# Kernel tuning notes

Measured on AMD Instinct MI355X. Metric: run time of the kernel, lower is better.

Reference implementation:

```python
import jax, jax.numpy as jnp
import numpy as np

N = 50000        # nodes
N_EDGES = 800000 # edges before self loops
D_IN = 128       # in_features
D_OUT = 64       # out_features (per head)
H = 2            # heads
NEG_SLOPE = 0.2  # GATv2Conv default negative_slope
EPS = 1e-5       # LayerNorm eps


def setup_inputs() -> dict:
    key = jax.random.key(0)
    ks = jax.random.split(key, 8)
    X = jax.random.normal(ks[0], (N, D_IN), jnp.float32)
    E = jax.random.randint(ks[1], (2, N_EDGES), 0, N, dtype=jnp.int32)
    attr = jax.random.normal(ks[2], (N_EDGES,), jnp.float32)
    # GATv2Conv params: lin_l / lin_r (share_weights=False, bias=True), att, concat bias
    s_in = 1.0 / np.sqrt(D_IN)
    W_l = jax.random.normal(ks[3], (D_IN, H * D_OUT), jnp.float32) * s_in
    b_l = jnp.zeros((H * D_OUT,), jnp.float32)
    W_r = jax.random.normal(ks[4], (D_IN, H * D_OUT), jnp.float32) * s_in
    b_r = jnp.zeros((H * D_OUT,), jnp.float32)
    att = jax.random.normal(ks[5], (H, D_OUT), jnp.float32) * (1.0 / np.sqrt(D_OUT))
    bias = jnp.zeros((H * D_OUT,), jnp.float32)
    # final_linear + LayerNorm params
    W_f = jax.random.normal(ks[6], (H * D_OUT, D_OUT), jnp.float32) * (1.0 / np.sqrt(H * D_OUT))
    b_f = jnp.zeros((D_OUT,), jnp.float32)
    gamma = jnp.ones((D_OUT,), jnp.float32)
    beta = jnp.zeros((D_OUT,), jnp.float32)
    return dict(X=X, E=E, attr=attr, W_l=W_l, b_l=b_l, W_r=W_r, b_r=b_r,
                att=att, bias=bias, W_f=W_f, b_f=b_f, gamma=gamma, beta=beta)


def _forward(X, E, W_l, b_l, W_r, b_r, att, bias, W_f, b_f, gamma, beta):
    # add self loops (PyG GATv2Conv default add_self_loops=True)
    loop = jnp.arange(N, dtype=E.dtype)
    src = jnp.concatenate([E[0], loop])  # [Et]
    dst = jnp.concatenate([E[1], loop])  # [Et]
    x_l = (X @ W_l + b_l).reshape(N, H, D_OUT)  # source-side transform
    x_r = (X @ W_r + b_r).reshape(N, H, D_OUT)  # target-side transform
    # per-edge GATv2 score: a^T LeakyReLU(x_i + x_j)
    s = jax.nn.leaky_relu(x_l[src] + x_r[dst], NEG_SLOPE)      # [Et, H, C]
    alpha = jnp.einsum('ehc,hc->eh', s, att)                   # [Et, H]
    # segment softmax over incoming edges of each target node
    a_max = jax.ops.segment_max(alpha, dst, num_segments=N)    # [N, H]
    a_max = jnp.where(jnp.isfinite(a_max), a_max, 0.0)
    num = jnp.exp(alpha - a_max[dst])
    den = jax.ops.segment_sum(num, dst, num_segments=N)
    w = num / den[dst]                                         # [Et, H]
    # weighted scatter-aggregate of source messages
    out = jax.ops.segment_sum(x_l[src] * w[:, :, None], dst, num_segments=N)  # [N,H,C]
    out = out.reshape(N, H * D_OUT) + bias                     # concat heads + bias
    # final linear + LayerNorm
    h = out @ W_f + b_f                                        # [N, D_OUT]
    mu = jnp.mean(h, axis=-1, keepdims=True)
    var = jnp.mean((h - mu) ** 2, axis=-1, keepdims=True)
    return (h - mu) * jax.lax.rsqrt(var + EPS) * gamma + beta


def reference(X, E, attr, W_l, b_l, W_r, b_r, att, bias, W_f, b_f, gamma, beta):
    H_out = _forward(X, E, W_l, b_l, W_r, b_r, att, bias, W_f, b_f, gamma, beta)
    return (H_out, E, attr)
```

## Files before the change

### kernel.cpp

```cpp
#include <hip/hip_runtime.h>

typedef unsigned short u16;
typedef unsigned int   u32;


#define DIN   128
#define DOUT  64
#define HD    128
#define BCAP  64

typedef __attribute__((ext_vector_type(8))) _Float16 f16x8;
typedef __attribute__((ext_vector_type(2))) _Float16 h2;
typedef __attribute__((ext_vector_type(4))) float    f32x4;

union H2U { u32 u; h2 h; };
__device__ __forceinline__ h2  U2H(u32 u) { H2U x; x.u = u; return x.h; }
__device__ __forceinline__ u32 H2Ub(h2 h) { H2U x; x.h = h; return x.u; }

__device__ __forceinline__ u16 f2h(float f) {
    _Float16 h = (_Float16)f;
    u16 r; __builtin_memcpy(&r, &h, 2); return r;
}

__device__ __forceinline__ u32 pkmax(u32 a, u32 b) {
    u32 d;
    asm("v_pk_max_f16 %0, %1, %2" : "=v"(d) : "v"(a), "v"(b));
    return d;
}

__device__ __forceinline__ float fdot2f(h2 a, h2 b, float c) {
#if __has_builtin(__builtin_amdgcn_fdot2)
    return __builtin_amdgcn_fdot2(a, b, c, false);
#else
    return c + (float)a[0] * (float)b[0] + (float)a[1] * (float)b[1];
#endif
}

__global__ void prep_small(const float* __restrict__ Wl, const float* __restrict__ Wr,
                           const float* __restrict__ Wf,
                           u16* __restrict__ WTl, u16* __restrict__ WTr,
                           uint4* __restrict__ Wfp, int* __restrict__ count, int N)
{
    int i = blockIdx.x * 256 + threadIdx.x;
    if (i < N) { count[i] = 0; return; }
    int j = i - N;
    if (j < 16384) {
        int k = j >> 7, c = j & 127;
        WTl[c * 128 + k] = f2h(Wl[j]);
    } else if (j < 32768) {
        int t = j - 16384;
        int k = t >> 7, c = t & 127;
        WTr[c * 128 + k] = f2h(Wr[t]);
    } else if (j < 33792) {
        int t = j - 32768;
        int k4 = t >> 5, c = t & 31;
        const float* wrow = Wf + (size_t)(4 * k4) * DOUT;
        u32 a0 = (u32)f2h(wrow[c])              | ((u32)f2h(wrow[DOUT + c]) << 16);
        u32 a1 = (u32)f2h(wrow[2 * DOUT + c])   | ((u32)f2h(wrow[3 * DOUT + c]) << 16);
        u32 a2 = (u32)f2h(wrow[c + 32])         | ((u32)f2h(wrow[DOUT + c + 32]) << 16);
        u32 a3 = (u32)f2h(wrow[2 * DOUT + c + 32]) | ((u32)f2h(wrow[3 * DOUT + c + 32]) << 16);
        Wfp[t] = make_uint4(a0, a1, a2, a3);
    }
}

__global__ void edge_prep(const int* __restrict__ E, const float* __restrict__ attr,
                          int* __restrict__ count, u16* __restrict__ bucket,
                          float* __restrict__ out, int N, int NE)
{
    int i = blockIdx.x * 256 + threadIdx.x;
    if (i < NE) {
        int src = E[i];
        int dst = E[NE + i];
        if ((u32)dst >= (u32)N) dst = 0;
        if ((u32)src >= (u32)N) src = 0;
        int rank = atomicAdd(&count[dst], 1);
        if (rank < BCAP) bucket[(size_t)dst * BCAP + rank] = (u16)src;
    } else {
        int j = i - NE;
        const size_t base = (size_t)N * DOUT;
        if (j < 2 * NE) {
            out[base + j] = (float)E[j];
        } else {
            int t = j - 2 * NE;
            if (t < NE) out[base + 2 * (size_t)NE + t] = attr[t];
        }
    }
}

__global__ __launch_bounds__(256) void gemm1(
    const float* __restrict__ X,
    const u16* __restrict__ WTl, const float* __restrict__ bl,
    const u16* __restrict__ WTr, const float* __restrict__ br,
    u16* __restrict__ xl_p, u16* __restrict__ xr_p, int N)
{
    __shared__ u16 sX[64 * 136];
    __shared__ u16 sW[128 * 136];

    const int tid  = threadIdx.x;
    const int row0 = blockIdx.x * 64;
    const int cb   = blockIdx.y;
    const u16*   WT  = (cb == 0) ? WTl : WTr;
    const float* bia = (cb == 0) ? bl : br;

    for (int idx = tid; idx < 64 * 32; idx += 256) {
        int r  = idx >> 5;
        int k4 = (idx & 31) << 2;
        int gr = row0 + r;
        float4 v = make_float4(0.f, 0.f, 0.f, 0.f);
        if (gr < N) v = *(const float4*)(X + (size_t)gr * DIN + k4);
        u32 p0 = (u32)f2h(v.x) | ((u32)f2h(v.y) << 16);
        u32 p1 = (u32)f2h(v.z) | ((u32)f2h(v.w) << 16);
        *(uint2*)&sX[r * 136 + k4] = make_uint2(p0, p1);
    }
    for (int idx = tid; idx < 128 * 16; idx += 256) {
        int c  = idx >> 4;
        int k8 = (idx & 15) << 3;
        *(uint4*)&sW[c * 136 + k8] = *(const uint4*)&WT[c * 128 + k8];
    }
    __syncthreads();

    const int wv   = tid >> 6;
    const int lane = tid & 63;
    const int m    = lane & 15;
    const int quad = lane >> 4;

    f32x4 acc[8] = {};
    #pragma unroll
    for (int kc = 0; kc < 4; kc++) {
        f16x8 bx = *(const f16x8*)&sX[(wv * 16 + m) * 136 + kc * 32 + quad * 8];
        #pragma unroll
        for (int t = 0; t < 8; t++) {
            f16x8 aw = *(const f16x8*)&sW[(t * 16 + m) * 136 + kc * 32 + quad * 8];
            acc[t] = __builtin_amdgcn_mfma_f32_16x16x32_f16(aw, bx, acc[t], 0, 0, 0);
        }
    }

    const int gn = row0 + wv * 16 + m;
    if (gn < N) {
        u16* dst = (cb == 0) ? xl_p : xr_p;
        #pragma unroll
        for (int t = 0; t < 8; t++) {
            const int c0 = t * 16 + quad * 4;
            float4 bv = *(const float4*)(bia + c0);
            u32 p0 = (u32)f2h(acc[t][0] + bv.x) | ((u32)f2h(acc[t][1] + bv.y) << 16);
            u32 p1 = (u32)f2h(acc[t][2] + bv.z) | ((u32)f2h(acc[t][3] + bv.w) << 16);
            *(uint2*)(dst + (size_t)gn * HD + c0) = make_uint2(p0, p1);
        }
    }
}

template<int D>
__device__ __forceinline__ void edge_block(
    int myidx, int j, int sgbase, const char* xbase,
    const h2* xr2, const h2* at2, h2 c02,
    h2* acc2, float& lden)
{
    uint4 q[D];
    #pragma unroll
    for (int b = 0; b < D; b++) {
        u32 off = (u32)__shfl(myidx, sgbase + j + 2 * b) << 8;
        q[b] = *(const uint4*)(xbase + off);
    }
    float sh[D];
    #pragma unroll
    for (int b = 0; b < D; b++) {
        h2 v0 = U2H(q[b].x) + xr2[0];
        h2 v1 = U2H(q[b].y) + xr2[1];
        h2 v2 = U2H(q[b].z) + xr2[2];
        h2 v3 = U2H(q[b].w) + xr2[3];
        v0 = U2H(pkmax(H2Ub(v0), H2Ub(v0 * c02)));
        v1 = U2H(pkmax(H2Ub(v1), H2Ub(v1 * c02)));
        v2 = U2H(pkmax(H2Ub(v2), H2Ub(v2 * c02)));
        v3 = U2H(pkmax(H2Ub(v3), H2Ub(v3 * c02)));
        float s = fdot2f(v0, at2[0], 0.f);
        s = fdot2f(v1, at2[1], s);
        s = fdot2f(v2, at2[2], s);
        s = fdot2f(v3, at2[3], s);
        sh[b] = s;
    }
    #pragma unroll
    for (int m = 4; m; m >>= 1) {
        #pragma unroll
        for (int b = 0; b < D; b++) sh[b] += __shfl_xor(sh[b], m);
    }
    #pragma unroll
    for (int b = 0; b < D; b++) {
        float p = exp2f(sh[b]);
        lden += p;
        _Float16 ph = (_Float16)p;
        h2 p2 = {ph, ph};
        acc2[0] += p2 * U2H(q[b].x);
        acc2[1] += p2 * U2H(q[b].y);
        acc2[2] += p2 * U2H(q[b].z);
        acc2[3] += p2 * U2H(q[b].w);
    }
}

__global__ __launch_bounds__(256, 8) void edge_fused(
    const u16* __restrict__ xl_p, const u16* __restrict__ xr_p,
    const float* __restrict__ att, const float* __restrict__ bias,
    const uint4* __restrict__ Wfp, const float* __restrict__ bf,
    const float* __restrict__ gamma, const float* __restrict__ beta,
    const int* __restrict__ count, const u16* __restrict__ bucket,
    float* __restrict__ out, int N)
{
    __shared__ uint4 sWp[32 * 32];
    __shared__ u32   sAggU[8 * 64];

    const int tid = threadIdx.x;
    for (int idx = tid; idx < 1024; idx += 256) sWp[idx] = Wfp[idx];
    __syncthreads();

    const int l      = tid & 63;
    const int half   = tid >> 5;
    const int hl     = tid & 31;
    const int g16    = l & 15;
    const int ch0    = g16 * 8;
    const int sgsel  = (l >> 4) & 1;
    const int sgbase = (l & 32) + sgsel;
    const int n      = blockIdx.x * 8 + half;
    const bool active = (n < N);

    const h2 c02 = {(_Float16)0.2f, (_Float16)0.2f};
    h2 at2[4], xr2[4];
    {
        const float L2E = 1.44269504f;
        float4 a0 = *(const float4*)(att + ch0);
        float4 a1 = *(const float4*)(att + ch0 + 4);
        at2[0] = h2{(_Float16)(a0.x * L2E), (_Float16)(a0.y * L2E)};
        at2[1] = h2{(_Float16)(a0.z * L2E), (_Float16)(a0.w * L2E)};
        at2[2] = h2{(_Float16)(a1.x * L2E), (_Float16)(a1.y * L2E)};
        at2[3] = h2{(_Float16)(a1.z * L2E), (_Float16)(a1.w * L2E)};
        uint4 pr = make_uint4(0, 0, 0, 0);
        if (active) pr = *(const uint4*)(xr_p + (size_t)n * HD + ch0);
        xr2[0] = U2H(pr.x); xr2[1] = U2H(pr.y);
        xr2[2] = U2H(pr.z); xr2[3] = U2H(pr.w);
    }

    h2 acc2[4] = {};
    float lden = 0.f;

    int cnt_b = 0;
    if (active) {
        cnt_b = count[n];
        if (cnt_b < 0) cnt_b = 0;
        if (cnt_b > BCAP) cnt_b = BCAP;
    }
    const int cnt = active ? cnt_b + 1 : 0;
    const u16* mybkt = bucket + (size_t)(active ? n : 0) * BCAP;

    const char* xbase = (const char*)xl_p + ch0 * 2;

    int done = 0;
    while (done < cnt) {
        int chunk = cnt - done; if (chunk > 32) chunk = 32;
        int myidx = 0;
        if (hl < chunk) {
            int gj = done + hl;
            myidx = (gj < cnt_b) ? (int)mybkt[gj] : n;
        }
        int j = 0;
        for (; j + 16 <= chunk; j += 16)
            edge_block<8>(myidx, j, sgbase, xbase, xr2, at2, c02, acc2, lden);
        if (j + 8 <= chunk) {
            edge_block<4>(myidx, j, sgbase, xbase, xr2, at2, c02, acc2, lden);
            j += 8;
        }
        if (j + 4 <= chunk) {
            edge_block<2>(myidx, j, sgbase, xbase, xr2, at2, c02, acc2, lden);
            j += 4;
        }
        for (; j < chunk; j += 2) {
            u32 off = (u32)__shfl(myidx, sgbase + j) << 8;
            uint4 q = *(const uint4*)(xbase + off);
            h2 v0 = U2H(q.x) + xr2[0];
            h2 v1 = U2H(q.y) + xr2[1];
            h2 v2 = U2H(q.z) + xr2[2];
            h2 v3 = U2H(q.w) + xr2[3];
            v0 = U2H(pkmax(H2Ub(v0), H2Ub(v0 * c02)));
            v1 = U2H(pkmax(H2Ub(v1), H2Ub(v1 * c02)));
            v2 = U2H(pkmax(H2Ub(v2), H2Ub(v2 * c02)));
            v3 = U2H(pkmax(H2Ub(v3), H2Ub(v3 * c02)));
            float s = fdot2f(v0, at2[0], 0.f);
            s = fdot2f(v1, at2[1], s);
            s = fdot2f(v2, at2[2], s);
            s = fdot2f(v3, at2[3], s);
            #pragma unroll
            for (int m = 4; m; m >>= 1) s += __shfl_xor(s, m);
            float p = (j + sgsel < chunk) ? exp2f(s) : 0.f;
            lden += p;
            _Float16 ph = (_Float16)p;
            h2 p2 = {ph, ph};
            acc2[0] += p2 * U2H(q.x);
            acc2[1] += p2 * U2H(q.y);
            acc2[2] += p2 * U2H(q.z);
            acc2[3] += p2 * U2H(q.w);
        }
        done += chunk;
    }

    #pragma unroll
    for (int i = 0; i < 4; i++) {
        u32 o = (u32)__shfl_xor((int)H2Ub(acc2[i]), 16);
        acc2[i] = acc2[i] + U2H(o);
    }
    lden += __shfl_xor(lden, 16);

    float rl = 1.f / fmaxf(lden, 1e-30f);
    if (!(l & 16)) {
        float4 b0 = *(const float4*)(bias + ch0);
        float4 b1 = *(const float4*)(bias + ch0 + 4);
        uint4 w;
        w.x = (u32)f2h((float)acc2[0][0] * rl + b0.x) |
              ((u32)f2h((float)acc2[0][1] * rl + b0.y) << 16);
        w.y = (u32)f2h((float)acc2[1][0] * rl + b0.z) |
              ((u32)f2h((float)acc2[1][1] * rl + b0.w) << 16);
        w.z = (u32)f2h((float)acc2[2][0] * rl + b1.x) |
              ((u32)f2h((float)acc2[2][1] * rl + b1.y) << 16);
        w.w = (u32)f2h((float)acc2[3][0] * rl + b1.z) |
              ((u32)f2h((float)acc2[3][1] * rl + b1.w) << 16);
        *(uint4*)&sAggU[half * 64 + g16 * 4] = w;
    }
    asm volatile("s_waitcnt lgkmcnt(0)" ::: "memory");

    float h0 = bf[hl], h1 = bf[hl + 32];
    #pragma unroll 8
    for (int k4 = 0; k4 < 32; k4++) {
        uint4 wp = sWp[k4 * 32 + hl];
        uint2 ag = *(const uint2*)&sAggU[half * 64 + k4 * 2];
        h0 = fdot2f(U2H(ag.x), U2H(wp.x), h0);
        h0 = fdot2f(U2H(ag.y), U2H(wp.y), h0);
        h1 = fdot2f(U2H(ag.x), U2H(wp.z), h1);
        h1 = fdot2f(U2H(ag.y), U2H(wp.w), h1);
    }

    float s1r = h0 + h1, s2r = h0 * h0 + h1 * h1;
    #pragma unroll
    for (int m = 16; m; m >>= 1) { s1r += __shfl_xor(s1r, m); s2r += __shfl_xor(s2r, m); }
    float mu  = s1r * (1.f / 64.f);
    float var = s2r * (1.f / 64.f) - mu * mu;
    float rs  = rsqrtf(fmaxf(var, 0.f) + 1e-5f);
    if (active) {
        out[(size_t)n * DOUT + hl]      = (h0 - mu) * rs * gamma[hl]      + beta[hl];
        out[(size_t)n * DOUT + hl + 32] = (h1 - mu) * rs * gamma[hl + 32] + beta[hl + 32];
    }
}

extern "C" void kernel_launch(void* const* d_in, const int* in_sizes, int n_in,
                              void* d_out, int out_size, void* d_ws, size_t ws_size,
                              hipStream_t stream) {
    const float* X    = (const float*)d_in[0];
    const int*   E    = (const int*)d_in[1];
    const float* attr = (const float*)d_in[2];
    const float* Wl   = (const float*)d_in[3];
    const float* bl   = (const float*)d_in[4];
    const float* Wr   = (const float*)d_in[5];
    const float* br   = (const float*)d_in[6];
    const float* att  = (const float*)d_in[7];
    const float* bias = (const float*)d_in[8];
    const float* Wf   = (const float*)d_in[9];
    const float* bf   = (const float*)d_in[10];
    const float* gamma= (const float*)d_in[11];
    const float* beta = (const float*)d_in[12];
    float* out = (float*)d_out;

    const int N  = in_sizes[0] / DIN;
    const int NE = in_sizes[1] / 2;

    char* ws = (char*)d_ws;
    int* count      = (int*)ws;               ws += (size_t)N * 4;
    u16* bucket     = (u16*)ws;               ws += (size_t)N * BCAP * 2;
    u16* xl_p       = (u16*)ws;               ws += (size_t)N * HD * 2;
    u16* xr_p       = (u16*)ws;               ws += (size_t)N * HD * 2;
    u16* WTl        = (u16*)ws;               ws += 128 * 128 * 2;
    u16* WTr        = (u16*)ws;               ws += 128 * 128 * 2;
    uint4* Wfp      = (uint4*)ws;             ws += 1024 * 16;

    prep_small<<<(N + 33792 + 255) / 256, 256, 0, stream>>>(
        Wl, Wr, Wf, WTl, WTr, Wfp, count, N);

    edge_prep<<<(4 * NE + 255) / 256, 256, 0, stream>>>(
        E, attr, count, bucket, out, N, NE);

    gemm1<<<dim3((N + 63) / 64, 2), 256, 0, stream>>>(X, WTl, bl, WTr, br, xl_p, xr_p, N);

    edge_fused<<<(N + 7) / 8, 256, 0, stream>>>(
        xl_p, xr_p, att, bias, Wfp, bf, gamma, beta,
        count, bucket, out, N);
}
```

Before: 223.1 us.

## Split edge scatter into destination-range passes, merge gemm halves, drop LDS weights

The edge bucket scatter now runs as four launches, each handling only edges whose destination falls in one quarter of the node range. The intent is to keep atomic counters and bucket writes within a cache-resident region, at the cost of reading the edge list four times. The output copy of E/attr moves into the prep kernel. gemm1 now computes both the left and right projections in one block, reusing the X tile and reading weights straight from global memory instead of staging them in LDS. The edge kernel's occupancy hint is lowered from 8 to 6 blocks per CU.

```diff
diff --git a/kernel.cpp b/kernel.cpp
--- a/kernel.cpp
+++ b/kernel.cpp
@@ -8,6 +8,7 @@
 #define DOUT  64
 #define HD    128
 #define BCAP  64
+#define NSEG  4
 
 typedef __attribute__((ext_vector_type(8))) _Float16 f16x8;
 typedef __attribute__((ext_vector_type(2))) _Float16 h2;
@@ -36,10 +37,12 @@
 #endif
 }
 
-__global__ void prep_small(const float* __restrict__ Wl, const float* __restrict__ Wr,
-                           const float* __restrict__ Wf,
-                           u16* __restrict__ WTl, u16* __restrict__ WTr,
-                           uint4* __restrict__ Wfp, int* __restrict__ count, int N)
+__global__ void k_prep(const float* __restrict__ Wl, const float* __restrict__ Wr,
+                       const float* __restrict__ Wf, const int* __restrict__ E,
+                       const float* __restrict__ attr,
+                       u16* __restrict__ WTl, u16* __restrict__ WTr,
+                       uint4* __restrict__ Wfp, int* __restrict__ count,
+                       float* __restrict__ out, int N, int NE)
 {
     int i = blockIdx.x * 256 + threadIdx.x;
     if (i < N) { count[i] = 0; return; }
@@ -60,31 +63,26 @@
         u32 a2 = (u32)f2h(wrow[c + 32])         | ((u32)f2h(wrow[DOUT + c + 32]) << 16);
         u32 a3 = (u32)f2h(wrow[2 * DOUT + c + 32]) | ((u32)f2h(wrow[3 * DOUT + c + 32]) << 16);
         Wfp[t] = make_uint4(a0, a1, a2, a3);
-    }
-}
-
-__global__ void edge_prep(const int* __restrict__ E, const float* __restrict__ attr,
-                          int* __restrict__ count, u16* __restrict__ bucket,
-                          float* __restrict__ out, int N, int NE)
-{
-    int i = blockIdx.x * 256 + threadIdx.x;
-    if (i < NE) {
-        int src = E[i];
-        int dst = E[NE + i];
-        if ((u32)dst >= (u32)N) dst = 0;
-        if ((u32)src >= (u32)N) src = 0;
-        int rank = atomicAdd(&count[dst], 1);
-        if (rank < BCAP) bucket[(size_t)dst * BCAP + rank] = (u16)src;
     } else {
-        int j = i - NE;
+        int p = j - 33792;
         const size_t base = (size_t)N * DOUT;
-        if (j < 2 * NE) {
-            out[base + j] = (float)E[j];
-        } else {
-            int t = j - 2 * NE;
-            if (t < NE) out[base + 2 * (size_t)NE + t] = attr[t];
-        }
-    }
+        if (p < 2 * NE)      out[base + p] = (float)E[p];
+        else if (p < 3 * NE) out[base + p] = attr[p - 2 * NE];
+    }
+}
+
+__global__ void k_scatter(const int* __restrict__ E, int* __restrict__ count,
+                          u16* __restrict__ bucket, int N, int NE, int lo, int hi)
+{
+    int e = blockIdx.x * 256 + threadIdx.x;
+    if (e >= NE) return;
+    int dst = E[NE + e];
+    if ((u32)dst >= (u32)N) dst = 0;
+    if (dst < lo || dst >= hi) return;
+    int src = E[e];
+    if ((u32)src >= (u32)N) src = 0;
+    int rank = atomicAdd(&count[dst], 1);
+    if (rank < BCAP) bucket[(size_t)dst * BCAP + rank] = (u16)src;
 }
 
 __global__ __launch_bounds__(256) void gemm1(
@@ -94,13 +92,9 @@
     u16* __restrict__ xl_p, u16* __restrict__ xr_p, int N)
 {
     __shared__ u16 sX[64 * 136];
-    __shared__ u16 sW[128 * 136];
 
     const int tid  = threadIdx.x;
     const int row0 = blockIdx.x * 64;
-    const int cb   = blockIdx.y;
-    const u16*   WT  = (cb == 0) ? WTl : WTr;
-    const float* bia = (cb == 0) ? bl : br;
 
     for (int idx = tid; idx < 64 * 32; idx += 256) {
         int r  = idx >> 5;
@@ -112,11 +106,6 @@
         u32 p1 = (u32)f2h(v.z) | ((u32)f2h(v.w) << 16);
         *(uint2*)&sX[r * 136 + k4] = make_uint2(p0, p1);
     }
-    for (int idx = tid; idx < 128 * 16; idx += 256) {
-        int c  = idx >> 4;
-        int k8 = (idx & 15) << 3;
-        *(uint4*)&sW[c * 136 + k8] = *(const uint4*)&WT[c * 128 + k8];
-    }
     __syncthreads();
 
     const int wv   = tid >> 6;
@@ -124,27 +113,36 @@
     const int m    = lane & 15;
     const int quad = lane >> 4;
 
-    f32x4 acc[8] = {};
-    #pragma unroll
-    for (int kc = 0; kc < 4; kc++) {
-        f16x8 bx = *(const f16x8*)&sX[(wv * 16 + m) * 136 + kc * 32 + quad * 8];
+    f16x8 bx[4];
+    #pragma unroll
+    for (int kc = 0; kc < 4; kc++)
+        bx[kc] = *(const f16x8*)&sX[(wv * 16 + m) * 136 + kc * 32 + quad * 8];
+
+    const int gn = row0 + wv * 16 + m;
+
+    #pragma unroll
+    for (int cb = 0; cb < 2; cb++) {
+        const u16*   WT  = cb ? WTr : WTl;
+        const float* bia = cb ? br  : bl;
+        f32x4 acc[8] = {};
         #pragma unroll
-        for (int t = 0; t < 8; t++) {
-            f16x8 aw = *(const f16x8*)&sW[(t * 16 + m) * 136 + kc * 32 + quad * 8];
-            acc[t] = __builtin_amdgcn_mfma_f32_16x16x32_f16(aw, bx, acc[t], 0, 0, 0);
-        }
-    }
-
-    const int gn = row0 + wv * 16 + m;
-    if (gn < N) {
-        u16* dst = (cb == 0) ? xl_p : xr_p;
-        #pragma unroll
-        for (int t = 0; t < 8; t++) {
-            const int c0 = t * 16 + quad * 4;
-            float4 bv = *(const float4*)(bia + c0);
-            u32 p0 = (u32)f2h(acc[t][0] + bv.x) | ((u32)f2h(acc[t][1] + bv.y) << 16);
-            u32 p1 = (u32)f2h(acc[t][2] + bv.z) | ((u32)f2h(acc[t][3] + bv.w) << 16);
-            *(uint2*)(dst + (size_t)gn * HD + c0) = make_uint2(p0, p1);
+        for (int kc = 0; kc < 4; kc++) {
+            #pragma unroll
+            for (int t = 0; t < 8; t++) {
+                f16x8 aw = *(const f16x8*)&WT[(t * 16 + m) * 128 + kc * 32 + quad * 8];
+                acc[t] = __builtin_amdgcn_mfma_f32_16x16x32_f16(aw, bx[kc], acc[t], 0, 0, 0);
+            }
+        }
+        if (gn < N) {
+            u16* dst = cb ? xr_p : xl_p;
+            #pragma unroll
+            for (int t = 0; t < 8; t++) {
+                const int c0 = t * 16 + quad * 4;
+                float4 bv = *(const float4*)(bia + c0);
+                u32 p0 = (u32)f2h(acc[t][0] + bv.x) | ((u32)f2h(acc[t][1] + bv.y) << 16);
+                u32 p1 = (u32)f2h(acc[t][2] + bv.z) | ((u32)f2h(acc[t][3] + bv.w) << 16);
+                *(uint2*)(dst + (size_t)gn * HD + c0) = make_uint2(p0, p1);
+            }
         }
     }
 }
@@ -196,7 +194,7 @@
     }
 }
 
-__global__ __launch_bounds__(256, 8) void edge_fused(
+__global__ __launch_bounds__(256, 6) void k_edge(
     const u16* __restrict__ xl_p, const u16* __restrict__ xr_p,
     const float* __restrict__ att, const float* __restrict__ bias,
     const uint4* __restrict__ Wfp, const float* __restrict__ bf,
@@ -204,7 +202,7 @@
     const int* __restrict__ count, const u16* __restrict__ bucket,
     float* __restrict__ out, int N)
 {
-    __shared__ uint4 sWp[32 * 32];
+    __shared__ uint4 sWp[1024];
     __shared__ u32   sAggU[8 * 64];
 
     const int tid = threadIdx.x;
@@ -366,6 +364,7 @@
 
     const int N  = in_sizes[0] / DIN;
     const int NE = in_sizes[1] / 2;
+    const int GB = (N + 63) / 64;
 
     char* ws = (char*)d_ws;
     int* count      = (int*)ws;               ws += (size_t)N * 4;
@@ -376,15 +375,19 @@
     u16* WTr        = (u16*)ws;               ws += 128 * 128 * 2;
     uint4* Wfp      = (uint4*)ws;             ws += 1024 * 16;
 
-    prep_small<<<(N + 33792 + 255) / 256, 256, 0, stream>>>(
-        Wl, Wr, Wf, WTl, WTr, Wfp, count, N);
-
-    edge_prep<<<(4 * NE + 255) / 256, 256, 0, stream>>>(
-        E, attr, count, bucket, out, N, NE);
-
-    gemm1<<<dim3((N + 63) / 64, 2), 256, 0, stream>>>(X, WTl, bl, WTr, br, xl_p, xr_p, N);
-
-    edge_fused<<<(N + 7) / 8, 256, 0, stream>>>(
-        xl_p, xr_p, att, bias, Wfp, bf, gamma, beta,
-        count, bucket, out, N);
-}
+    const int prep_items = N + 33792 + 3 * NE;
+    k_prep<<<(prep_items + 255) / 256, 256, 0, stream>>>(
+        Wl, Wr, Wf, E, attr, WTl, WTr, Wfp, count, out, N, NE);
+
+    for (int s = 0; s < NSEG; s++) {
+        int lo = (int)((long long)s * N / NSEG);
+        int hi = (int)((long long)(s + 1) * N / NSEG);
+        k_scatter<<<(NE + 255) / 256, 256, 0, stream>>>(
+            E, count, bucket, N, NE, lo, hi);
+    }
+
+    gemm1<<<GB, 256, 0, stream>>>(X, WTl, bl, WTr, br, xl_p, xr_p, N);
+
+    k_edge<<<(N + 7) / 8, 256, 0, stream>>>(
+        xl_p, xr_p, att, bias, Wfp, bf, gamma, beta, count, bucket, out, N);
+}
```

Result: slower. 244.5 us (+9.6%).
